# Performance work log

Measured on AMD Instinct MI355X. Metric: run time of the kernel, lower is better.

## Reference

```python
import jax, jax.numpy as jnp
import numpy as np

EPS = 1e-5  # BatchNorm eps; eval mode with default running stats (mean=0, var=1)


def _bn(h, gamma, beta):
    # eval-mode BatchNorm2d with running_mean=0, running_var=1
    scale = gamma / jnp.sqrt(1.0 + EPS)
    return h * scale[None, :, None, None] + beta[None, :, None, None]


def _conv1x1(h, w, b):
    # 1x1 conv == channel matmul. h: [B,C,H,W], w: [O,C], b: [O]
    return jnp.einsum('bchw,oc->bohw', h, w) + b[None, :, None, None]


def setup_inputs() -> dict:
    key = jax.random.key(0)
    ks = jax.random.split(key, 16)
    B, C, H, W = 8, 64, 64, 64
    inp = {
        'x': jax.random.normal(ks[0], (B, C, H, W), dtype=jnp.float32),
        'saliency_map': jax.random.uniform(ks[1], (B, H, W), dtype=jnp.float32),
    }
    i = 2
    for name in ('q', 'k', 'v'):
        inp[f'w_{name}'] = jax.random.normal(ks[i], (C, C), dtype=jnp.float32) * (1.0 / np.sqrt(C)); i += 1
        inp[f'b_{name}'] = jax.random.normal(ks[i], (C,), dtype=jnp.float32) * 0.02; i += 1
        inp[f'g_{name}'] = 1.0 + 0.1 * jax.random.normal(ks[i], (C,), dtype=jnp.float32); i += 1
        inp[f'be_{name}'] = jax.random.normal(ks[i], (C,), dtype=jnp.float32) * 0.02; i += 1
    inp['g_o'] = 1.0 + 0.1 * jax.random.normal(ks[14], (C,), dtype=jnp.float32)
    inp['be_o'] = jax.random.normal(ks[15], (C,), dtype=jnp.float32) * 0.02
    return inp


def reference(x, saliency_map, w_q, b_q, g_q, be_q, w_k, b_k, g_k, be_k,
              w_v, b_v, g_v, be_v, g_o, be_o):
    B, C, H, W = x.shape
    HW = H * W
    query = _bn(_conv1x1(x, w_q, b_q), g_q, be_q).reshape(B, C, HW)
    key_ = _bn(_conv1x1(x, w_k, b_k), g_k, be_k).reshape(B, C, HW)
    value = _bn(_conv1x1(x, w_v, b_v), g_v, be_v).reshape(B, C, HW)
    mask = saliency_map.reshape(B, 1, HW)  # broadcast over channels == repeat
    query = query * mask
    # scores[b,i,j] = sum_c q[b,c,i] * k[b,c,j]; softmax over j (no scaling)
    scores = jnp.einsum('bci,bcj->bij', query, key_)
    attn = jax.nn.softmax(scores, axis=-1)
    # out[b,c,j] = sum_i v[b,c,i] * attn[b,i,j]
    enhanced = jnp.einsum('bci,bij->bcj', value, attn).reshape(B, C, H, W)
    enhanced = enhanced + x
    return _bn(enhanced, g_o, be_o)
```

## Files before the change

kernel.cpp:

```cpp
#include <hip/hip_runtime.h>

#define EPS 1e-5f
#define LOG2E 1.4426950408889634f

typedef __attribute__((ext_vector_type(8)))  short    s8b;
typedef __attribute__((ext_vector_type(4)))  short    s4b;
typedef __attribute__((ext_vector_type(16))) float    f32x16;
typedef __attribute__((ext_vector_type(4)))  float    f32x4;
typedef __attribute__((ext_vector_type(4)))  unsigned u32x4;

__device__ __forceinline__ unsigned cvt_pk_bf16(float lo, float hi) {
    unsigned r;
    asm("v_cvt_pk_bf16_f32 %0, %1, %2" : "=v"(r) : "v"(lo), "v"(hi));
    return r;
}
__device__ __forceinline__ void permswap(unsigned &a, unsigned &b) {
    asm("v_permlane32_swap_b32 %0, %1" : "+v"(a), "+v"(b));
}
union PackAB { u32x4 u; s8b s; };

__device__ __forceinline__ unsigned short f2bf(float f) {
    union { float f; unsigned u; } v; v.f = f;
    unsigned r = v.u + 0x7FFFu + ((v.u >> 16) & 1u);
    return (unsigned short)(r >> 16);
}
__device__ __forceinline__ float bf2f(unsigned short h) {
    union { unsigned u; float f; } v; v.u = ((unsigned)h) << 16;
    return v.f;
}


__global__ __launch_bounds__(256) void qkv_kernel(
    const float* __restrict__ x, const float* __restrict__ sal,
    const float* __restrict__ wq, const float* __restrict__ bq,
    const float* __restrict__ gq, const float* __restrict__ beq,
    const float* __restrict__ wk, const float* __restrict__ bk,
    const float* __restrict__ gk, const float* __restrict__ bek,
    const float* __restrict__ wv, const float* __restrict__ bv,
    const float* __restrict__ gv, const float* __restrict__ bev,
    short* __restrict__ Qf, short* __restrict__ Kf, short* __restrict__ Vf)
{
    __shared__ short wbf[6][4096];
    __shared__ short xbf[4096];
    __shared__ short v_lds[4096];
    __shared__ float sc_lds[3][64];
    __shared__ float bb_lds[3][64];

    const int t = threadIdx.x;
    const int b = blockIdx.x & 7;
    const int p0 = (blockIdx.x >> 3) * 64;

    if (t < 192) {
        int m = t >> 6, o = t & 63;
        const float* g  = (m == 0) ? gq  : (m == 1) ? gk  : gv;
        const float* be = (m == 0) ? beq : (m == 1) ? bek : bev;
        const float* bi = (m == 0) ? bq  : (m == 1) ? bk  : bv;
        float lam = (m == 0) ? LOG2E : 1.0f;
        float s = g[o] * rsqrtf(1.0f + EPS) * lam;
        sc_lds[m][o] = s;
        bb_lds[m][o] = bi[o] * s + be[o] * lam;
    }
    __syncthreads();

    for (int rep = 0; rep < 12; ++rep) {
        int idx = (rep * 256 + t) * 4;
        int m = idx >> 12;
        int r = idx & 4095;
        int o = r >> 6, c0 = r & 63;
        const float* w = (m == 0) ? wq : (m == 1) ? wk : wv;
        float4 v4 = *reinterpret_cast<const float4*>(w + r);
        float s = sc_lds[m][o];
        float w0 = v4.x * s, w1 = v4.y * s, w2 = v4.z * s, w3 = v4.w * s;
        unsigned short h0 = f2bf(w0), h1 = f2bf(w1), h2 = f2bf(w2), h3 = f2bf(w3);
        s4b hv, lv;
        hv[0] = (short)h0; hv[1] = (short)h1; hv[2] = (short)h2; hv[3] = (short)h3;
        lv[0] = (short)f2bf(w0 - bf2f(h0));
        lv[1] = (short)f2bf(w1 - bf2f(h1));
        lv[2] = (short)f2bf(w2 - bf2f(h2));
        lv[3] = (short)f2bf(w3 - bf2f(h3));
        int sidx = (o * 64 + c0) ^ ((o & 7) << 3);
        *reinterpret_cast<s4b*>(&wbf[m * 2 + 0][sidx]) = hv;
        *reinterpret_cast<s4b*>(&wbf[m * 2 + 1][sidx]) = lv;
    }
    {
        const int xp = t & 63;
        const int cgrp = (t >> 6) * 4;
        const float* xb = x + ((size_t)(b * 64) << 12) + p0 + xp;
        for (int rep = 0; rep < 4; ++rep) {
            int cb = cgrp + rep * 16;
            float x0 = xb[(size_t)(cb + 0) << 12];
            float x1 = xb[(size_t)(cb + 1) << 12];
            float x2 = xb[(size_t)(cb + 2) << 12];
            float x3 = xb[(size_t)(cb + 3) << 12];
            s4b pk;
            pk[0] = (short)f2bf(x0); pk[1] = (short)f2bf(x1);
            pk[2] = (short)f2bf(x2); pk[3] = (short)f2bf(x3);
            int sidx = (xp * 64 + cb) ^ ((xp & 7) << 3);
            *reinterpret_cast<s4b*>(&xbf[sidx]) = pk;
        }
    }
    __syncthreads();

    const int lane = t & 63, wave = t >> 6;
    const int l31 = lane & 31, hi = lane >> 5;
    const int phalf = wave & 1, ohalf = wave >> 1;
    const int prow = phalf * 32 + l31;
    const int orow = ohalf * 32 + l31;
    const int ib = (p0 >> 5) + phalf;
    const int swz = (l31 & 7) << 3;

    s8b bx[4];
#pragma unroll
    for (int s = 0; s < 4; ++s)
        bx[s] = *reinterpret_cast<const s8b*>(
            &xbf[(prow * 64 + s * 16 + hi * 8) ^ ((prow & 7) << 3)]);

    const float msk = sal[(((size_t)b) << 12) + p0 + prow];

#pragma unroll
    for (int m = 0; m < 3; ++m) {
        s8b ah[4], al[4];
#pragma unroll
        for (int s = 0; s < 4; ++s) {
            int sidx = (orow * 64 + s * 16 + hi * 8) ^ swz;
            ah[s] = *reinterpret_cast<const s8b*>(&wbf[m * 2 + 0][sidx]);
            al[s] = *reinterpret_cast<const s8b*>(&wbf[m * 2 + 1][sidx]);
        }
        f32x16 d;
#pragma unroll
        for (int r = 0; r < 16; ++r) d[r] = 0.f;
#pragma unroll
        for (int s = 0; s < 4; ++s)
            d = __builtin_amdgcn_mfma_f32_32x32x16_bf16(ah[s], bx[s], d, 0, 0, 0);
#pragma unroll
        for (int s = 0; s < 4; ++s)
            d = __builtin_amdgcn_mfma_f32_32x32x16_bf16(al[s], bx[s], d, 0, 0, 0);

        float pv[16];
#pragma unroll
        for (int g = 0; g < 4; ++g) {
            f32x4 bb = *reinterpret_cast<const f32x4*>(
                &bb_lds[m][ohalf * 32 + 8 * g + 4 * hi]);
#pragma unroll
            for (int q = 0; q < 4; ++q) pv[g * 4 + q] = d[g * 4 + q] + bb[q];
        }
        if (m == 0) {
#pragma unroll
            for (int r = 0; r < 16; ++r) pv[r] *= msk;
        }
        if (m < 2) {
            unsigned a0 = cvt_pk_bf16(pv[0],  pv[1]);
            unsigned a1 = cvt_pk_bf16(pv[2],  pv[3]);
            unsigned a2 = cvt_pk_bf16(pv[4],  pv[5]);
            unsigned a3 = cvt_pk_bf16(pv[6],  pv[7]);
            unsigned b0 = cvt_pk_bf16(pv[8],  pv[9]);
            unsigned b1 = cvt_pk_bf16(pv[10], pv[11]);
            unsigned b2 = cvt_pk_bf16(pv[12], pv[13]);
            unsigned b3 = cvt_pk_bf16(pv[14], pv[15]);
            permswap(a0, a2); permswap(a1, a3);
            permswap(b0, b2); permswap(b1, b3);
            PackAB pa0, pa1;
            pa0.u.x = a0; pa0.u.y = a1; pa0.u.z = a2; pa0.u.w = a3;
            pa1.u.x = b0; pa1.u.y = b1; pa1.u.z = b2; pa1.u.w = b3;
            short* dst = (m == 0) ? Qf : Kf;
            size_t base =
                ((((size_t)(b * 128 + ib) * 4 + ohalf * 2) * 2 + hi) * 32 + l31) * 8;
            *reinterpret_cast<u32x4*>(dst + base)       = pa0.u;
            *reinterpret_cast<u32x4*>(dst + base + 512) = pa1.u;
        } else {
#pragma unroll
            for (int r = 0; r < 16; ++r) {
                int c = ohalf * 32 + (r & 3) + 8 * (r >> 2) + 4 * hi;
                int sidx = (c * 64 + prow) ^ ((c & 7) << 3);
                v_lds[sidx] = (short)f2bf(pv[r]);
            }
        }
    }
    __syncthreads();

    const size_t vbase = (size_t)(b * 128 + (p0 >> 5)) * 2048;
#pragma unroll
    for (int r = 0; r < 2; ++r) {
        int f = r * 256 + t;
        int c = f & 63;
        int iL = ((f >> 6) & 7) * 8;
        int sidx = (c * 64 + iL) ^ ((c & 7) << 3);
        u32x4 val = *reinterpret_cast<const u32x4*>(&v_lds[sidx]);
        *reinterpret_cast<u32x4*>(Vf + vbase + (size_t)f * 8) = val;
    }
}

#define LOADK(JB, DST) {                                                      \
    const short* _kp = Kf +                                                   \
        ((((size_t)(b * 128 + (JB)) * 4) * 2 + hi) * 32 + l31) * 8;           \
    DST[0] = *reinterpret_cast<const s8b*>(_kp);                              \
    DST[1] = *reinterpret_cast<const s8b*>(_kp + 512);                        \
    DST[2] = *reinterpret_cast<const s8b*>(_kp + 1024);                       \
    DST[3] = *reinterpret_cast<const s8b*>(_kp + 1536); }

#define RBODY(KARR) {                                                         \
    f32x16 sacc;                                                              \
    _Pragma("unroll") for (int r = 0; r < 16; ++r) sacc[r] = 0.f;             \
    __builtin_amdgcn_s_setprio(1);                                            \
    _Pragma("unroll") for (int s = 0; s < 4; ++s)                             \
        sacc = __builtin_amdgcn_mfma_f32_32x32x16_bf16(qf[s], KARR[s], sacc, 0, 0, 0); \
    __builtin_amdgcn_s_setprio(0);                                            \
    _Pragma("unroll") for (int r = 0; r < 16; ++r)                            \
        lsum[r] += __builtin_exp2f(sacc[r]); }

__global__ __launch_bounds__(256, 4) void rowsum_kernel(
    const short* __restrict__ Qf, const short* __restrict__ Kf,
    float* __restrict__ inv_l)
{
    __shared__ float part[4][32];

    const int t = threadIdx.x;
    const int b = blockIdx.x & 7;
    const int it = blockIdx.x >> 3;
    const int wave = t >> 6, lane = t & 63;
    const int l31 = lane & 31, hi = lane >> 5;

    const short* qp = Qf +
        ((((size_t)(b * 128 + it) * 4) * 2 + hi) * 32 + l31) * 8;
    s8b qf[4];
#pragma unroll
    for (int s = 0; s < 4; ++s)
        qf[s] = *reinterpret_cast<const s8b*>(qp + s * 512);

    float lsum[16];
#pragma unroll
    for (int r = 0; r < 16; ++r) lsum[r] = 0.f;

    s8b kA[4], kB[4];
    LOADK(wave, kA);
    for (int ii = 0; ii < 32; ii += 2) {
        LOADK(wave + (ii + 1) * 4, kB);
        RBODY(kA);
        if (ii + 2 < 32) { LOADK(wave + (ii + 2) * 4, kA); }
        RBODY(kB);
    }

#pragma unroll
    for (int off = 1; off < 32; off <<= 1)
#pragma unroll
        for (int r = 0; r < 16; ++r) lsum[r] += __shfl_xor(lsum[r], off);

    if (l31 == 0) {
#pragma unroll
        for (int r = 0; r < 16; ++r) {
            int iloc = (r & 3) + 8 * (r >> 2) + 4 * hi;
            part[wave][iloc] = lsum[r];
        }
    }
    __syncthreads();
    if (t < 32)
        inv_l[(((size_t)b) << 12) + it * 32 + t] =
            1.0f / (part[0][t] + part[1][t] + part[2][t] + part[3][t]);
}

#define LOADQ(IB, DST) {                                                      \
    const short* _qp = Qf +                                                   \
        ((((size_t)(b * 128 + (IB)) * 4) * 2 + hi) * 32 + l31) * 8;           \
    DST[0] = *reinterpret_cast<const s8b*>(_qp);                              \
    DST[1] = *reinterpret_cast<const s8b*>(_qp + 512);                        \
    DST[2] = *reinterpret_cast<const s8b*>(_qp + 1024);                       \
    DST[3] = *reinterpret_cast<const s8b*>(_qp + 1536); }

#define LOADV(IB) {                                                           \
    const short* _vp = Vf +                                                   \
        ((((size_t)(b * 128 + (IB)) * 2) * 2 + hi) * 64 + l31) * 8;           \
    vf[0] = *reinterpret_cast<const s8b*>(_vp);                               \
    vf[1] = *reinterpret_cast<const s8b*>(_vp + 256);                         \
    vf[2] = *reinterpret_cast<const s8b*>(_vp + 1024);                        \
    vf[3] = *reinterpret_cast<const s8b*>(_vp + 1280); }

#define ABODY(QARR, IB) {                                                     \
    f32x16 sacc;                                                              \
    _Pragma("unroll") for (int r = 0; r < 16; ++r) sacc[r] = 0.f;             \
    __builtin_amdgcn_s_setprio(1);                                            \
    _Pragma("unroll") for (int s = 0; s < 4; ++s)                             \
        sacc = __builtin_amdgcn_mfma_f32_32x32x16_bf16(QARR[s], kf[s], sacc, 0, 0, 0); \
    __builtin_amdgcn_s_setprio(0);                                            \
    float p[16];                                                              \
    const int _ibase = (IB) * 32 + 4 * hi;                                    \
    _Pragma("unroll") for (int g = 0; g < 4; ++g) {                           \
        f32x4 li = *reinterpret_cast<const f32x4*>(lip + _ibase + 8 * g);     \
        _Pragma("unroll") for (int q = 0; q < 4; ++q)                         \
            p[g * 4 + q] = __builtin_exp2f(sacc[g * 4 + q]) * li[q];          \
    }                                                                         \
    unsigned a0 = cvt_pk_bf16(p[0],  p[1]),  a1 = cvt_pk_bf16(p[2],  p[3]);   \
    unsigned a2 = cvt_pk_bf16(p[4],  p[5]),  a3 = cvt_pk_bf16(p[6],  p[7]);   \
    unsigned b0 = cvt_pk_bf16(p[8],  p[9]),  b1 = cvt_pk_bf16(p[10], p[11]);  \
    unsigned b2 = cvt_pk_bf16(p[12], p[13]), b3 = cvt_pk_bf16(p[14], p[15]);  \
    permswap(a0, a2); permswap(a1, a3); permswap(b0, b2); permswap(b1, b3);   \
    PackAB pa0, pa1;                                                          \
    pa0.u.x = a0; pa0.u.y = a1; pa0.u.z = a2; pa0.u.w = a3;                   \
    pa1.u.x = b0; pa1.u.y = b1; pa1.u.z = b2; pa1.u.w = b3;                   \
    __builtin_amdgcn_s_setprio(1);                                            \
    acc0 = __builtin_amdgcn_mfma_f32_32x32x16_bf16(pa0.s, vf[0], acc0, 0, 0, 0); \
    acc1 = __builtin_amdgcn_mfma_f32_32x32x16_bf16(pa0.s, vf[1], acc1, 0, 0, 0); \
    acc0 = __builtin_amdgcn_mfma_f32_32x32x16_bf16(pa1.s, vf[2], acc0, 0, 0, 0); \
    acc1 = __builtin_amdgcn_mfma_f32_32x32x16_bf16(pa1.s, vf[3], acc1, 0, 0, 0); \
    __builtin_amdgcn_s_setprio(0); }

__global__ __launch_bounds__(256, 4) void attnout_kernel(
    const short* __restrict__ Qf, const short* __restrict__ Kf,
    const short* __restrict__ Vf, const float* __restrict__ inv_l,
    const float* __restrict__ x, const float* __restrict__ go,
    const float* __restrict__ beo, float* __restrict__ out)
{
    __shared__ float red[3][64][33];

    const int t = threadIdx.x;
    const int b = blockIdx.x & 7;
    const int jb = blockIdx.x >> 3;
    const int wave = t >> 6, lane = t & 63;
    const int wr = wave;
    const int l31 = lane & 31, hi = lane >> 5;

    const short* kp = Kf +
        ((((size_t)(b * 128 + jb) * 4) * 2 + hi) * 32 + l31) * 8;
    s8b kf[4];
#pragma unroll
    for (int s = 0; s < 4; ++s)
        kf[s] = *reinterpret_cast<const s8b*>(kp + s * 512);

    f32x16 acc0, acc1;
#pragma unroll
    for (int r = 0; r < 16; ++r) { acc0[r] = 0.f; acc1[r] = 0.f; }

    const float* lip = inv_l + (((size_t)b) << 12);

    s8b qA[4], qB[4], vf[4];
    LOADQ(wr, qA);
    LOADV(wr);
    for (int ii = 0; ii < 32; ii += 2) {
        const int ibA = ii * 4 + wr;
        const int ibB = ibA + 4;
        LOADQ(ibB, qB);
        ABODY(qA, ibA);
        LOADV(ibB);
        if (ii + 2 < 32) { LOADQ(ibA + 8, qA); }
        ABODY(qB, ibB);
        if (ii + 2 < 32) { LOADV(ibA + 8); }
    }

    if (wr > 0) {
#pragma unroll
        for (int nf = 0; nf < 2; ++nf) {
            const f32x16& A = nf ? acc1 : acc0;
            int c = nf * 32 + l31;
#pragma unroll
            for (int g = 0; g < 4; ++g) {
                f32x4 v;
                v.x = A[g * 4 + 0]; v.y = A[g * 4 + 1];
                v.z = A[g * 4 + 2]; v.w = A[g * 4 + 3];
                *reinterpret_cast<f32x4*>(&red[wr - 1][c][g * 8 + 4 * hi]) = v;
            }
        }
    }
    __syncthreads();
    if (wr == 0) {
#pragma unroll
        for (int nf = 0; nf < 2; ++nf) {
            const f32x16& A = nf ? acc1 : acc0;
            int c = nf * 32 + l31;
            const float sc = go[c] * rsqrtf(1.0f + EPS);
            const float bb = beo[c];
            size_t rowb = (((size_t)(b * 64 + c)) << 12) + jb * 32;
#pragma unroll
            for (int g = 0; g < 4; ++g) {
                int jl = g * 8 + 4 * hi;
                f32x4 p0 = *reinterpret_cast<const f32x4*>(&red[0][c][jl]);
                f32x4 p1 = *reinterpret_cast<const f32x4*>(&red[1][c][jl]);
                f32x4 p2 = *reinterpret_cast<const f32x4*>(&red[2][c][jl]);
                f32x4 xv = *reinterpret_cast<const f32x4*>(x + rowb + jl);
                f32x4 ov;
                ov.x = (A[g * 4 + 0] + p0.x + p1.x + p2.x + xv.x) * sc + bb;
                ov.y = (A[g * 4 + 1] + p0.y + p1.y + p2.y + xv.y) * sc + bb;
                ov.z = (A[g * 4 + 2] + p0.z + p1.z + p2.z + xv.z) * sc + bb;
                ov.w = (A[g * 4 + 3] + p0.w + p1.w + p2.w + xv.w) * sc + bb;
                *reinterpret_cast<f32x4*>(out + rowb + jl) = ov;
            }
        }
    }
}

extern "C" void kernel_launch(void* const* d_in, const int* in_sizes, int n_in,
                              void* d_out, int out_size, void* d_ws, size_t ws_size,
                              hipStream_t stream)
{
    (void)in_sizes; (void)n_in; (void)out_size; (void)ws_size;
    const float* x   = (const float*)d_in[0];
    const float* sal = (const float*)d_in[1];
    const float* wq  = (const float*)d_in[2];  const float* bq  = (const float*)d_in[3];
    const float* gq  = (const float*)d_in[4];  const float* beq = (const float*)d_in[5];
    const float* wk  = (const float*)d_in[6];  const float* bk  = (const float*)d_in[7];
    const float* gk  = (const float*)d_in[8];  const float* bek = (const float*)d_in[9];
    const float* wv  = (const float*)d_in[10]; const float* bv  = (const float*)d_in[11];
    const float* gv  = (const float*)d_in[12]; const float* bev = (const float*)d_in[13];
    const float* go  = (const float*)d_in[14]; const float* beo = (const float*)d_in[15];
    float* out = (float*)d_out;

    short* ws = (short*)d_ws;
    short* Qf = ws;
    short* Kf = ws + 2097152;
    short* Vf = ws + 4194304;
    float* il = (float*)(ws + 6291456);

    qkv_kernel<<<512, 256, 0, stream>>>(x, sal, wq, bq, gq, beq,
                                        wk, bk, gk, bek, wv, bv, gv, bev,
                                        Qf, Kf, Vf);
    rowsum_kernel<<<1024, 256, 0, stream>>>(Qf, Kf, il);
    attnout_kernel<<<1024, 256, 0, stream>>>(Qf, Kf, Vf, il, x, go, beo, out);
}
```

Before: 222.6 us.

## Use 512-thread blocks covering two tiles so paired waves share K/Q/V loads

Both the rowsum and attention-output kernels now launch 512-thread blocks that each handle two 32-row/column tiles, with waves split into two groups. The aim is better cache reuse, since the paired waves stream the same K (rowsum) or Q/V (attnout) tiles together, and half as many blocks are launched. V loads are also double-buffered like Q, so the next V tile is fetched before the current body runs. The cost is extra register pressure from the added V buffer, a larger shared-memory reduction array, and different occupancy under the launch bounds.

```diff
diff --git a/kernel.cpp b/kernel.cpp
--- a/kernel.cpp
+++ b/kernel.cpp
@@ -208,20 +208,21 @@
     _Pragma("unroll") for (int r = 0; r < 16; ++r)                            \
         lsum[r] += __builtin_exp2f(sacc[r]); }
 
-__global__ __launch_bounds__(256, 4) void rowsum_kernel(
+__global__ __launch_bounds__(512, 2) void rowsum_kernel(
     const short* __restrict__ Qf, const short* __restrict__ Kf,
     float* __restrict__ inv_l)
 {
-    __shared__ float part[4][32];
+    __shared__ float part[8][32];
 
     const int t = threadIdx.x;
     const int b = blockIdx.x & 7;
-    const int it = blockIdx.x >> 3;
+    const int it2 = blockIdx.x >> 3;
     const int wave = t >> 6, lane = t & 63;
+    const int wi = wave & 1, wj = wave >> 1;
     const int l31 = lane & 31, hi = lane >> 5;
 
     const short* qp = Qf +
-        ((((size_t)(b * 128 + it) * 4) * 2 + hi) * 32 + l31) * 8;
+        ((((size_t)(b * 128 + it2 * 2 + wi) * 4) * 2 + hi) * 32 + l31) * 8;
     s8b qf[4];
 #pragma unroll
     for (int s = 0; s < 4; ++s)
@@ -232,11 +233,11 @@
     for (int r = 0; r < 16; ++r) lsum[r] = 0.f;
 
     s8b kA[4], kB[4];
-    LOADK(wave, kA);
-    for (int ii = 0; ii < 32; ii += 2) {
-        LOADK(wave + (ii + 1) * 4, kB);
+    LOADK(wj, kA);
+    for (int jj = 0; jj < 32; jj += 2) {
+        LOADK((jj + 1) * 4 + wj, kB);
         RBODY(kA);
-        if (ii + 2 < 32) { LOADK(wave + (ii + 2) * 4, kA); }
+        if (jj + 2 < 32) { LOADK((jj + 2) * 4 + wj, kA); }
         RBODY(kB);
     }
 
@@ -253,9 +254,12 @@
         }
     }
     __syncthreads();
-    if (t < 32)
-        inv_l[(((size_t)b) << 12) + it * 32 + t] =
-            1.0f / (part[0][t] + part[1][t] + part[2][t] + part[3][t]);
+    if (t < 64) {
+        int wi_t = t >> 5, row = t & 31;
+        float s = part[wi_t][row] + part[2 + wi_t][row] +
+                  part[4 + wi_t][row] + part[6 + wi_t][row];
+        inv_l[(((size_t)b) << 12) + it2 * 64 + wi_t * 32 + row] = 1.0f / s;
+    }
 }
 
 #define LOADQ(IB, DST) {                                                      \
@@ -266,15 +270,15 @@
     DST[2] = *reinterpret_cast<const s8b*>(_qp + 1024);                       \
     DST[3] = *reinterpret_cast<const s8b*>(_qp + 1536); }
 
-#define LOADV(IB) {                                                           \
+#define LOADV(IB, DST) {                                                      \
     const short* _vp = Vf +                                                   \
         ((((size_t)(b * 128 + (IB)) * 2) * 2 + hi) * 64 + l31) * 8;           \
-    vf[0] = *reinterpret_cast<const s8b*>(_vp);                               \
-    vf[1] = *reinterpret_cast<const s8b*>(_vp + 256);                         \
-    vf[2] = *reinterpret_cast<const s8b*>(_vp + 1024);                        \
-    vf[3] = *reinterpret_cast<const s8b*>(_vp + 1280); }
-
-#define ABODY(QARR, IB) {                                                     \
+    DST[0] = *reinterpret_cast<const s8b*>(_vp);                              \
+    DST[1] = *reinterpret_cast<const s8b*>(_vp + 256);                        \
+    DST[2] = *reinterpret_cast<const s8b*>(_vp + 1024);                       \
+    DST[3] = *reinterpret_cast<const s8b*>(_vp + 1280); }
+
+#define ABODY(QARR, VARR, IB) {                                               \
     f32x16 sacc;                                                              \
     _Pragma("unroll") for (int r = 0; r < 16; ++r) sacc[r] = 0.f;             \
     __builtin_amdgcn_s_setprio(1);                                            \
@@ -297,29 +301,30 @@
     pa0.u.x = a0; pa0.u.y = a1; pa0.u.z = a2; pa0.u.w = a3;                   \
     pa1.u.x = b0; pa1.u.y = b1; pa1.u.z = b2; pa1.u.w = b3;                   \
     __builtin_amdgcn_s_setprio(1);                                            \
-    acc0 = __builtin_amdgcn_mfma_f32_32x32x16_bf16(pa0.s, vf[0], acc0, 0, 0, 0); \
-    acc1 = __builtin_amdgcn_mfma_f32_32x32x16_bf16(pa0.s, vf[1], acc1, 0, 0, 0); \
-    acc0 = __builtin_amdgcn_mfma_f32_32x32x16_bf16(pa1.s, vf[2], acc0, 0, 0, 0); \
-    acc1 = __builtin_amdgcn_mfma_f32_32x32x16_bf16(pa1.s, vf[3], acc1, 0, 0, 0); \
+    acc0 = __builtin_amdgcn_mfma_f32_32x32x16_bf16(pa0.s, VARR[0], acc0, 0, 0, 0); \
+    acc1 = __builtin_amdgcn_mfma_f32_32x32x16_bf16(pa0.s, VARR[1], acc1, 0, 0, 0); \
+    acc0 = __builtin_amdgcn_mfma_f32_32x32x16_bf16(pa1.s, VARR[2], acc0, 0, 0, 0); \
+    acc1 = __builtin_amdgcn_mfma_f32_32x32x16_bf16(pa1.s, VARR[3], acc1, 0, 0, 0); \
     __builtin_amdgcn_s_setprio(0); }
 
-__global__ __launch_bounds__(256, 4) void attnout_kernel(
+__global__ __launch_bounds__(512, 2) void attnout_kernel(
     const short* __restrict__ Qf, const short* __restrict__ Kf,
     const short* __restrict__ Vf, const float* __restrict__ inv_l,
     const float* __restrict__ x, const float* __restrict__ go,
     const float* __restrict__ beo, float* __restrict__ out)
 {
-    __shared__ float red[3][64][33];
+    __shared__ float red[2][3][64][33];
 
     const int t = threadIdx.x;
     const int b = blockIdx.x & 7;
-    const int jb = blockIdx.x >> 3;
+    const int jt = blockIdx.x >> 3;
     const int wave = t >> 6, lane = t & 63;
-    const int wr = wave;
+    const int wr = wave >> 1;
+    const int wc = wave & 1;
     const int l31 = lane & 31, hi = lane >> 5;
 
     const short* kp = Kf +
-        ((((size_t)(b * 128 + jb) * 4) * 2 + hi) * 32 + l31) * 8;
+        ((((size_t)(b * 128 + jt * 2 + wc) * 4) * 2 + hi) * 32 + l31) * 8;
     s8b kf[4];
 #pragma unroll
     for (int s = 0; s < 4; ++s)
@@ -331,18 +336,17 @@
 
     const float* lip = inv_l + (((size_t)b) << 12);
 
-    s8b qA[4], qB[4], vf[4];
+    s8b qA[4], qB[4], vA[4], vB[4];
     LOADQ(wr, qA);
-    LOADV(wr);
+    LOADV(wr, vA);
     for (int ii = 0; ii < 32; ii += 2) {
         const int ibA = ii * 4 + wr;
         const int ibB = ibA + 4;
         LOADQ(ibB, qB);
-        ABODY(qA, ibA);
-        LOADV(ibB);
-        if (ii + 2 < 32) { LOADQ(ibA + 8, qA); }
-        ABODY(qB, ibB);
-        if (ii + 2 < 32) { LOADV(ibA + 8); }
+        LOADV(ibB, vB);
+        ABODY(qA, vA, ibA);
+        if (ii + 2 < 32) { LOADQ(ibA + 8, qA); LOADV(ibA + 8, vA); }
+        ABODY(qB, vB, ibB);
     }
 
     if (wr > 0) {
@@ -355,7 +359,7 @@
                 f32x4 v;
                 v.x = A[g * 4 + 0]; v.y = A[g * 4 + 1];
                 v.z = A[g * 4 + 2]; v.w = A[g * 4 + 3];
-                *reinterpret_cast<f32x4*>(&red[wr - 1][c][g * 8 + 4 * hi]) = v;
+                *reinterpret_cast<f32x4*>(&red[wc][wr - 1][c][g * 8 + 4 * hi]) = v;
             }
         }
     }
@@ -367,13 +371,13 @@
             int c = nf * 32 + l31;
             const float sc = go[c] * rsqrtf(1.0f + EPS);
             const float bb = beo[c];
-            size_t rowb = (((size_t)(b * 64 + c)) << 12) + jb * 32;
+            size_t rowb = (((size_t)(b * 64 + c)) << 12) + jt * 64 + wc * 32;
 #pragma unroll
             for (int g = 0; g < 4; ++g) {
                 int jl = g * 8 + 4 * hi;
-                f32x4 p0 = *reinterpret_cast<const f32x4*>(&red[0][c][jl]);
-                f32x4 p1 = *reinterpret_cast<const f32x4*>(&red[1][c][jl]);
-                f32x4 p2 = *reinterpret_cast<const f32x4*>(&red[2][c][jl]);
+                f32x4 p0 = *reinterpret_cast<const f32x4*>(&red[wc][0][c][jl]);
+                f32x4 p1 = *reinterpret_cast<const f32x4*>(&red[wc][1][c][jl]);
+                f32x4 p2 = *reinterpret_cast<const f32x4*>(&red[wc][2][c][jl]);
                 f32x4 xv = *reinterpret_cast<const f32x4*>(x + rowb + jl);
                 f32x4 ov;
                 ov.x = (A[g * 4 + 0] + p0.x + p1.x + p2.x + xv.x) * sc + bb;
@@ -411,6 +415,6 @@
     qkv_kernel<<<512, 256, 0, stream>>>(x, sal, wq, bq, gq, beq,
                                         wk, bk, gk, bek, wv, bv, gv, bev,
                                         Qf, Kf, Vf);
-    rowsum_kernel<<<1024, 256, 0, stream>>>(Qf, Kf, il);
-    attnout_kernel<<<1024, 256, 0, stream>>>(Qf, Kf, Vf, il, x, go, beo, out);
-}
+    rowsum_kernel<<<512, 512, 0, stream>>>(Qf, Kf, il);
+    attnout_kernel<<<512, 512, 0, stream>>>(Qf, Kf, Vf, il, x, go, beo, out);
+}
```

Measured after the change: 199.9 us. -10.2%, faster.
